# Optimization experiments

Measured on AMD Instinct MI355X. Metric: run time of the kernel, lower is better.

Reference implementation:

```python
import jax, jax.numpy as jnp
import numpy as np

N_ATT, N_HEAD, D_K, D_IN = 4, 8, 64, 512
B, T = 128, 512
TEMP = float(np.sqrt(D_K))  # temperature = d_k ** 0.5


def setup_inputs() -> dict:
    key = jax.random.key(0)
    k1, k2, k3 = jax.random.split(key, 3)
    v = jax.random.normal(k1, (B, T, D_IN), jnp.float32)
    # nn.Parameter Q init: normal(0, sqrt(2/d_k))
    Q = jax.random.normal(k2, (N_ATT, N_HEAD, D_K), jnp.float32) * np.sqrt(2.0 / D_K)
    # fc1_k: Linear(d_in, num_attention*n_head*d_k), weight ~ N(0, sqrt(2/d_k))
    Wk = jax.random.normal(k3, (N_ATT * N_HEAD * D_K, D_IN), jnp.float32) * np.sqrt(2.0 / D_K)
    bk = jnp.zeros((N_ATT * N_HEAD * D_K,), jnp.float32)
    return {"v": v, "Q": Q, "Wk": Wk, "bk": bk}


def reference(v, Q, Wk, bk):
    A, H, dk = Q.shape
    Bsz, Tt, d_in = v.shape
    c = d_in // H  # per-head value channels

    # q = stack(Q, dim=2 over batch).view(-1, d_k)  -> [A*H*B, d_k]
    q = jnp.broadcast_to(Q[:, :, None, :], (A, H, Bsz, dk)).reshape(-1, dk)

    # k = fc1_k(v).view(B,T,A,H,dk).permute(3,0,1,2,4).contiguous().view(-1,T,dk)
    # NOTE: this view is a raw C-order reinterpretation (scrambles t/A axes);
    # transpose + reshape reproduces torch's contiguous().view() exactly.
    k = (v @ Wk.T + bk).reshape(Bsz, Tt, A, H, dk)
    k = jnp.transpose(k, (3, 0, 1, 2, 4)).reshape(-1, Tt, dk)  # [H*B*A, T, dk]

    # v heads: stack(v.split(c, dim=-1)).view(H*B, T, c)
    vh = jnp.transpose(v.reshape(Bsz, Tt, H, c), (2, 0, 1, 3)).reshape(H * Bsz, Tt, c)

    # single-query scaled dot-product attention (dropout in eval mode -> identity)
    attn = jnp.einsum('xd,xtd->xt', q, k) / TEMP  # [A*H*B, T]
    attn = jax.nn.softmax(attn, axis=-1)

    # v[:, None].expand(-1, A, -1, -1).reshape(-1, T, c)
    vexp = jnp.broadcast_to(vh[:, None], (H * Bsz, A, Tt, c)).reshape(-1, Tt, c)
    out = jnp.einsum('xt,xtc->xc', attn, vexp)  # [A*H*B, c]

    output = out.reshape(A, H, Bsz, c)
    attn = attn.reshape(A, H, Bsz, Tt)
    return output, attn
```

## Files before the change

kernel.cpp:

```cpp
#include <hip/hip_runtime.h>
#include <hip/hip_bf16.h>
#include <math.h>

#define DIN 512
#define TT  512

using bf16x8 = __attribute__((ext_vector_type(8))) short;
using f32x4  = __attribute__((ext_vector_type(4))) float;

static __device__ __forceinline__ unsigned short f2bf(float x) {
    __hip_bfloat16 h = __float2bfloat16(x);
    return *reinterpret_cast<unsigned short*>(&h);
}
static __device__ __forceinline__ unsigned int pack2(float a, float b) {
    return (unsigned int)f2bf(a) | ((unsigned int)f2bf(b) << 16);
}


__global__ __launch_bounds__(512) void pk_kernel(const float* __restrict__ Q,
                                                 const float* __restrict__ Wk,
                                                 const float* __restrict__ bk,
                                                 unsigned short* __restrict__ Pgb,
                                                 float* __restrict__ qb) {
    const int bid = blockIdx.x;
    const int bg = bid >> 5;
    const int p  = bid & 31;
    const int h  = p >> 2;
    const int ua = p & 3;
    const int a_q = h >> 1;
    const int h_q = (4 * h + bg) & 7;
    const int ch_base = ua * 512 + h * 64;

    __shared__ float qv[64];
    const int tid = threadIdx.x;
    if (tid < 64) qv[tid] = Q[(a_q * 8 + h_q) * 64 + tid];
    __syncthreads();

    const int s = tid;
    float acc = 0.f;
    #pragma unroll 8
    for (int d = 0; d < 64; ++d)
        acc += qv[d] * Wk[(size_t)(ch_base + d) * DIN + s];
    Pgb[(size_t)(bg * 32 + p) * 512 + s] = f2bf(acc * 0.125f);

    if (tid == 0) {
        float sum = 0.f;
        for (int d = 0; d < 64; ++d) sum += qv[d] * bk[ch_base + d];
        qb[bg * 32 + p] = sum * 0.125f;
    }
}

__global__ __launch_bounds__(256) void score_kernel(const float* __restrict__ v,
                                                    const unsigned short* __restrict__ Pgb,
                                                    const float* __restrict__ qb,
                                                    float* __restrict__ attn) {
    const int bid = blockIdx.x;
    const int b = bid >> 2;
    const int j = bid & 3;
    const int bg = b >> 5;
    const int tid = threadIdx.x;
    const int lane = tid & 63;
    const int w = tid >> 6;

    __shared__ __align__(16) char VtB[2][128 * 80];
    __shared__ float red2[4][2][4][2];

    const float* vbase = v + ((size_t)b * TT + j * 128) * DIN;
    const int srow  = tid >> 1;
    const int shalf = tid & 1;
    const float* vsrc = vbase + (size_t)srow * DIN + shalf * 16;
    const int vdo = srow * 80 + shalf * 32;

    const unsigned short* pb0 = Pgb + ((size_t)(bg * 32) + (lane & 15)) * 512 + (lane >> 4) * 8;
    const unsigned short* pb1 = pb0 + 16 * 512;

    const int akb = (lane >> 4) * 16;
    const int aoff = (w * 32 + (lane & 15)) * 80 + akb;

    const float qv0 = qb[bg * 32 + (lane & 15)];
    const float qv1 = qb[bg * 32 + 16 + (lane & 15)];

    f32x4 acc[2][2];
    #pragma unroll
    for (int i = 0; i < 2; ++i)
        #pragma unroll
        for (int n = 0; n < 2; ++n)
            #pragma unroll
            for (int r = 0; r < 4; ++r) acc[i][n][r] = 0.f;

    float4 vrA[4], vrB[4];
    bf16x8 brA0, brA1, brB0, brB1;
    #pragma unroll
    for (int q = 0; q < 4; ++q) vrA[q] = *(const float4*)(vsrc + q * 4);
    brA0 = *(const bf16x8*)(pb0);
    brA1 = *(const bf16x8*)(pb1);
    {
        uint4 lo, hi;
        lo.x = pack2(vrA[0].x, vrA[0].y); lo.y = pack2(vrA[0].z, vrA[0].w);
        lo.z = pack2(vrA[1].x, vrA[1].y); lo.w = pack2(vrA[1].z, vrA[1].w);
        hi.x = pack2(vrA[2].x, vrA[2].y); hi.y = pack2(vrA[2].z, vrA[2].w);
        hi.z = pack2(vrA[3].x, vrA[3].y); hi.w = pack2(vrA[3].z, vrA[3].w);
        *(uint4*)(VtB[0] + vdo)      = lo;
        *(uint4*)(VtB[0] + vdo + 16) = hi;
    }
    __syncthreads();

#define STEP(CUR, VRN, BRC0, BRC1, BRN0, BRN1, KT)                            \
    {                                                                         \
        if ((KT) + 1 < 16) {                                                  \
            const float* vn = vsrc + ((KT) + 1) * 32;                         \
            VRN[0] = *(const float4*)(vn);                                    \
            VRN[1] = *(const float4*)(vn + 4);                                \
            VRN[2] = *(const float4*)(vn + 8);                                \
            VRN[3] = *(const float4*)(vn + 12);                               \
            BRN0 = *(const bf16x8*)(pb0 + ((KT) + 1) * 32);                   \
            BRN1 = *(const bf16x8*)(pb1 + ((KT) + 1) * 32);                   \
        }                                                                     \
        bf16x8 a0 = *(const bf16x8*)(VtB[CUR] + aoff);                        \
        bf16x8 a1 = *(const bf16x8*)(VtB[CUR] + aoff + 16 * 80);              \
        acc[0][0] = __builtin_amdgcn_mfma_f32_16x16x32_bf16(a0, BRC0, acc[0][0], 0, 0, 0); \
        acc[0][1] = __builtin_amdgcn_mfma_f32_16x16x32_bf16(a0, BRC1, acc[0][1], 0, 0, 0); \
        acc[1][0] = __builtin_amdgcn_mfma_f32_16x16x32_bf16(a1, BRC0, acc[1][0], 0, 0, 0); \
        acc[1][1] = __builtin_amdgcn_mfma_f32_16x16x32_bf16(a1, BRC1, acc[1][1], 0, 0, 0); \
        if ((KT) + 1 < 16) {                                                  \
            uint4 lo, hi;                                                     \
            lo.x = pack2(VRN[0].x, VRN[0].y); lo.y = pack2(VRN[0].z, VRN[0].w); \
            lo.z = pack2(VRN[1].x, VRN[1].y); lo.w = pack2(VRN[1].z, VRN[1].w); \
            hi.x = pack2(VRN[2].x, VRN[2].y); hi.y = pack2(VRN[2].z, VRN[2].w); \
            hi.z = pack2(VRN[3].x, VRN[3].y); hi.w = pack2(VRN[3].z, VRN[3].w); \
            *(uint4*)(VtB[(CUR) ^ 1] + vdo)      = lo;                        \
            *(uint4*)(VtB[(CUR) ^ 1] + vdo + 16) = hi;                        \
        }                                                                     \
        __syncthreads();                                                      \
    }

    for (int kt = 0; kt < 16; kt += 2) {
        STEP(0, vrB, brA0, brA1, brB0, brB1, kt)
        STEP(1, vrA, brB0, brB1, brA0, brA1, kt + 1)
    }
#undef STEP

    float lg[2][8];
    #pragma unroll
    for (int i = 0; i < 2; ++i)
        #pragma unroll
        for (int r = 0; r < 4; ++r) {
            lg[0][i * 4 + r] = acc[i][0][r] + qv0;
            lg[1][i * 4 + r] = acc[i][1][r] + qv1;
        }

    const int hsub = (lane >> 2) & 3;
    float mw[2], sw[2], ev[2][8];
    #pragma unroll
    for (int nt = 0; nt < 2; ++nt) {
        float m = lg[nt][0];
        #pragma unroll
        for (int q = 1; q < 8; ++q) m = fmaxf(m, lg[nt][q]);
        m = fmaxf(m, __shfl_xor(m, 1));
        m = fmaxf(m, __shfl_xor(m, 2));
        m = fmaxf(m, __shfl_xor(m, 16));
        m = fmaxf(m, __shfl_xor(m, 32));
        float s = 0.f;
        #pragma unroll
        for (int q = 0; q < 8; ++q) { ev[nt][q] = __expf(lg[nt][q] - m); s += ev[nt][q]; }
        s += __shfl_xor(s, 1);
        s += __shfl_xor(s, 2);
        s += __shfl_xor(s, 16);
        s += __shfl_xor(s, 32);
        mw[nt] = m; sw[nt] = s;
    }
    if ((lane & 0x33) == 0) {
        #pragma unroll
        for (int nt = 0; nt < 2; ++nt) {
            red2[w][nt][hsub][0] = mw[nt];
            red2[w][nt][hsub][1] = sw[nt];
        }
    }
    __syncthreads();

    #pragma unroll
    for (int nt = 0; nt < 2; ++nt) {
        float M = red2[0][nt][hsub][0];
        M = fmaxf(M, red2[1][nt][hsub][0]);
        M = fmaxf(M, red2[2][nt][hsub][0]);
        M = fmaxf(M, red2[3][nt][hsub][0]);
        float S = 0.f;
        #pragma unroll
        for (int w2 = 0; w2 < 4; ++w2)
            S += __expf(red2[w2][nt][hsub][0] - M) * red2[w2][nt][hsub][1];
        const float factor = __expf(mw[nt] - M) / S;

        const int h = nt * 4 + hsub;
        float* arow = attn + ((size_t)(h * 512 + b * 4 + j)) * 512;
        const int ua = lane & 3;
        #pragma unroll
        for (int i = 0; i < 2; ++i)
            #pragma unroll
            for (int r = 0; r < 4; ++r) {
                const int trow = w * 32 + i * 16 + ((lane >> 4) & 3) * 4 + r;
                arow[trow * 4 + ua] = ev[nt][i * 4 + r] * factor;
            }
    }
}

__global__ __launch_bounds__(256) void pv_kernel(const float* __restrict__ v,
                                                 const float* __restrict__ attn,
                                                 float* __restrict__ out) {
    const int bid = blockIdx.x;
    const int b = bid >> 3;
    const int h = bid & 7;
    const int tid = threadIdx.x;

    __shared__ __align__(16) char smem[34816];
    float (*at)[512]    = reinterpret_cast<float (*)[512]>(smem);
    float (*red)[4][68] = reinterpret_cast<float (*)[4][68]>(smem);

    {
        const int j  = tid >> 6;
        const int u8 = (tid & 63) * 8;
        const float* src = attn + ((size_t)(h * 512 + b * 4 + j)) * 512 + u8;
        *(float4*)&at[j][u8]     = *(const float4*)(src);
        *(float4*)&at[j][u8 + 4] = *(const float4*)(src + 4);
    }
    __syncthreads();

    const int cg = tid & 7;
    const int up = tid >> 3;
    const int c8 = cg * 8;
    const float* vb = v + (size_t)b * TT * DIN + h * 64 + c8;

    float acc[4][8];
    #pragma unroll
    for (int jj = 0; jj < 4; ++jj)
        #pragma unroll
        for (int ci = 0; ci < 8; ++ci) acc[jj][ci] = 0.f;

    float4 r0 = *(const float4*)(vb + (size_t)up * DIN);
    float4 r1 = *(const float4*)(vb + (size_t)up * DIN + 4);

    for (int it = 0; it < 16; ++it) {
        const int u = it * 32 + up;
        const float4 c0 = r0;
        const float4 c1 = r1;
        if (it < 15) {
            const float* pn = vb + (size_t)(u + 32) * DIN;
            r0 = *(const float4*)(pn);
            r1 = *(const float4*)(pn + 4);
        }
        const float a0 = at[0][u];
        const float a1 = at[1][u];
        const float a2 = at[2][u];
        const float a3 = at[3][u];
        acc[0][0] += a0 * c0.x; acc[0][1] += a0 * c0.y; acc[0][2] += a0 * c0.z; acc[0][3] += a0 * c0.w;
        acc[0][4] += a0 * c1.x; acc[0][5] += a0 * c1.y; acc[0][6] += a0 * c1.z; acc[0][7] += a0 * c1.w;
        acc[1][0] += a1 * c0.x; acc[1][1] += a1 * c0.y; acc[1][2] += a1 * c0.z; acc[1][3] += a1 * c0.w;
        acc[1][4] += a1 * c1.x; acc[1][5] += a1 * c1.y; acc[1][6] += a1 * c1.z; acc[1][7] += a1 * c1.w;
        acc[2][0] += a2 * c0.x; acc[2][1] += a2 * c0.y; acc[2][2] += a2 * c0.z; acc[2][3] += a2 * c0.w;
        acc[2][4] += a2 * c1.x; acc[2][5] += a2 * c1.y; acc[2][6] += a2 * c1.z; acc[2][7] += a2 * c1.w;
        acc[3][0] += a3 * c0.x; acc[3][1] += a3 * c0.y; acc[3][2] += a3 * c0.z; acc[3][3] += a3 * c0.w;
        acc[3][4] += a3 * c1.x; acc[3][5] += a3 * c1.y; acc[3][6] += a3 * c1.z; acc[3][7] += a3 * c1.w;
    }

    __syncthreads();

    #pragma unroll
    for (int jj = 0; jj < 4; ++jj) {
        float4 w0, w1;
        w0.x = acc[jj][0]; w0.y = acc[jj][1]; w0.z = acc[jj][2]; w0.w = acc[jj][3];
        w1.x = acc[jj][4]; w1.y = acc[jj][5]; w1.z = acc[jj][6]; w1.w = acc[jj][7];
        *(float4*)&red[up][jj][c8]     = w0;
        *(float4*)&red[up][jj][c8 + 4] = w1;
    }
    __syncthreads();

    const int jo = tid >> 6;
    const int c  = tid & 63;
    float s = 0.f;
    #pragma unroll
    for (int r2 = 0; r2 < 32; ++r2) s += red[r2][jo][c];
    out[((size_t)(h * 512 + b * 4 + jo)) * 64 + c] = s;
}

extern "C" void kernel_launch(void* const* d_in, const int* in_sizes, int n_in,
                              void* d_out, int out_size, void* d_ws, size_t ws_size,
                              hipStream_t stream) {
    const float* v  = (const float*)d_in[0];
    const float* Q  = (const float*)d_in[1];
    const float* Wk = (const float*)d_in[2];
    const float* bk = (const float*)d_in[3];

    float* out  = (float*)d_out;
    float* attn = out + 4096 * 64;

    unsigned short* Pgb = (unsigned short*)d_ws;
    float* qb = (float*)(Pgb + 4 * 32 * 512);

    pk_kernel<<<128, 512, 0, stream>>>(Q, Wk, bk, Pgb, qb);
    score_kernel<<<512, 256, 0, stream>>>(v, Pgb, qb, attn);
    pv_kernel<<<1024, 256, 0, stream>>>(v, attn, out);
}
```

Measured before the change: 59.17 us.

## Fuse score and PV kernels into persistent work-queue kernel with per-batch flags

```diff
diff --git a/kernel.cpp b/kernel.cpp
--- a/kernel.cpp
+++ b/kernel.cpp
@@ -21,7 +21,9 @@
                                                  const float* __restrict__ Wk,
                                                  const float* __restrict__ bk,
                                                  unsigned short* __restrict__ Pgb,
-                                                 float* __restrict__ qb) {
+                                                 float* __restrict__ qb,
+                                                 int* __restrict__ flags,
+                                                 int* __restrict__ ctr) {
     const int bid = blockIdx.x;
     const int bg = bid >> 5;
     const int p  = bid & 31;
@@ -34,6 +36,10 @@
     __shared__ float qv[64];
     const int tid = threadIdx.x;
     if (tid < 64) qv[tid] = Q[(a_q * 8 + h_q) * 64 + tid];
+    if (tid == 0) {
+        flags[bid] = 0;
+        if (bid == 0) *ctr = 0;
+    }
     __syncthreads();
 
     const int s = tid;
@@ -50,60 +56,75 @@
     }
 }
 
-__global__ __launch_bounds__(256) void score_kernel(const float* __restrict__ v,
-                                                    const unsigned short* __restrict__ Pgb,
-                                                    const float* __restrict__ qb,
-                                                    float* __restrict__ attn) {
-    const int bid = blockIdx.x;
-    const int b = bid >> 2;
-    const int j = bid & 3;
-    const int bg = b >> 5;
-    const int tid = threadIdx.x;
+__global__ __launch_bounds__(256, 3) void persist_kernel(
+        const float* __restrict__ v,
+        const unsigned short* __restrict__ Pgb,
+        const float* __restrict__ qb,
+        float* __restrict__ attn,
+        float* __restrict__ out,
+        int* __restrict__ flags,
+        int* __restrict__ ctr)
+{
+    __shared__ __align__(16) char smem[34816];
+    __shared__ int s_item;
+    const int tid  = threadIdx.x;
     const int lane = tid & 63;
-    const int w = tid >> 6;
-
-    __shared__ __align__(16) char VtB[2][128 * 80];
-    __shared__ float red2[4][2][4][2];
-
-    const float* vbase = v + ((size_t)b * TT + j * 128) * DIN;
-    const int srow  = tid >> 1;
-    const int shalf = tid & 1;
-    const float* vsrc = vbase + (size_t)srow * DIN + shalf * 16;
-    const int vdo = srow * 80 + shalf * 32;
-
-    const unsigned short* pb0 = Pgb + ((size_t)(bg * 32) + (lane & 15)) * 512 + (lane >> 4) * 8;
-    const unsigned short* pb1 = pb0 + 16 * 512;
-
-    const int akb = (lane >> 4) * 16;
-    const int aoff = (w * 32 + (lane & 15)) * 80 + akb;
-
-    const float qv0 = qb[bg * 32 + (lane & 15)];
-    const float qv1 = qb[bg * 32 + 16 + (lane & 15)];
-
-    f32x4 acc[2][2];
-    #pragma unroll
-    for (int i = 0; i < 2; ++i)
-        #pragma unroll
-        for (int n = 0; n < 2; ++n)
-            #pragma unroll
-            for (int r = 0; r < 4; ++r) acc[i][n][r] = 0.f;
-
-    float4 vrA[4], vrB[4];
-    bf16x8 brA0, brA1, brB0, brB1;
-    #pragma unroll
-    for (int q = 0; q < 4; ++q) vrA[q] = *(const float4*)(vsrc + q * 4);
-    brA0 = *(const bf16x8*)(pb0);
-    brA1 = *(const bf16x8*)(pb1);
-    {
-        uint4 lo, hi;
-        lo.x = pack2(vrA[0].x, vrA[0].y); lo.y = pack2(vrA[0].z, vrA[0].w);
-        lo.z = pack2(vrA[1].x, vrA[1].y); lo.w = pack2(vrA[1].z, vrA[1].w);
-        hi.x = pack2(vrA[2].x, vrA[2].y); hi.y = pack2(vrA[2].z, vrA[2].w);
-        hi.z = pack2(vrA[3].x, vrA[3].y); hi.w = pack2(vrA[3].z, vrA[3].w);
-        *(uint4*)(VtB[0] + vdo)      = lo;
-        *(uint4*)(VtB[0] + vdo + 16) = hi;
-    }
-    __syncthreads();
+    const int w    = tid >> 6;
+
+    for (;;) {
+        __syncthreads();
+        if (tid == 0) s_item = atomicAdd(ctr, 1);
+        __syncthreads();
+        const int item = s_item;
+        if (item >= 1536) break;
+
+        if (item < 512) {
+            const int b = item >> 2;
+            const int j = item & 3;
+            const int bg = b >> 5;
+
+            char* vt[2] = { smem, smem + 10240 };
+            float (*red2)[2][4][2] = reinterpret_cast<float (*)[2][4][2]>(smem + 20480);
+
+            const float* vbase = v + ((size_t)b * TT + j * 128) * DIN;
+            const int srow  = tid >> 1;
+            const int shalf = tid & 1;
+            const float* vsrc = vbase + (size_t)srow * DIN + shalf * 16;
+            const int vdo = srow * 80 + shalf * 32;
+
+            const unsigned short* pb0 = Pgb + ((size_t)(bg * 32) + (lane & 15)) * 512 + (lane >> 4) * 8;
+            const unsigned short* pb1 = pb0 + 16 * 512;
+
+            const int akb  = (lane >> 4) * 16;
+            const int aoff = (w * 32 + (lane & 15)) * 80 + akb;
+
+            const float qv0 = qb[bg * 32 + (lane & 15)];
+            const float qv1 = qb[bg * 32 + 16 + (lane & 15)];
+
+            f32x4 acc[2][2];
+            #pragma unroll
+            for (int i = 0; i < 2; ++i)
+                #pragma unroll
+                for (int n = 0; n < 2; ++n)
+                    #pragma unroll
+                    for (int r = 0; r < 4; ++r) acc[i][n][r] = 0.f;
+
+            float4 vrA[4], vrB[4];
+            bf16x8 brA0, brA1, brB0, brB1;
+            #pragma unroll
+            for (int q = 0; q < 4; ++q) vrA[q] = *(const float4*)(vsrc + q * 4);
+            brA0 = *(const bf16x8*)(pb0);
+            brA1 = *(const bf16x8*)(pb1);
+            {
+                uint4 lo, hi;
+                lo.x = pack2(vrA[0].x, vrA[0].y); lo.y = pack2(vrA[0].z, vrA[0].w);
+                lo.z = pack2(vrA[1].x, vrA[1].y); lo.w = pack2(vrA[1].z, vrA[1].w);
+                hi.x = pack2(vrA[2].x, vrA[2].y); hi.y = pack2(vrA[2].z, vrA[2].w);
+                hi.z = pack2(vrA[3].x, vrA[3].y); hi.w = pack2(vrA[3].z, vrA[3].w);
+                *(uint4*)(vt[0] + vdo)      = lo;
+                *(uint4*)(vt[0] + vdo + 16) = hi;
+            }
+            __syncthreads();
 
 #define STEP(CUR, VRN, BRC0, BRC1, BRN0, BRN1, KT)                            \
     {                                                                         \
@@ -116,8 +137,8 @@
             BRN0 = *(const bf16x8*)(pb0 + ((KT) + 1) * 32);                   \
             BRN1 = *(const bf16x8*)(pb1 + ((KT) + 1) * 32);                   \
         }                                                                     \
-        bf16x8 a0 = *(const bf16x8*)(VtB[CUR] + aoff);                        \
-        bf16x8 a1 = *(const bf16x8*)(VtB[CUR] + aoff + 16 * 80);              \
+        bf16x8 a0 = *(const bf16x8*)(vt[CUR] + aoff);                         \
+        bf16x8 a1 = *(const bf16x8*)(vt[CUR] + aoff + 16 * 80);               \
         acc[0][0] = __builtin_amdgcn_mfma_f32_16x16x32_bf16(a0, BRC0, acc[0][0], 0, 0, 0); \
         acc[0][1] = __builtin_amdgcn_mfma_f32_16x16x32_bf16(a0, BRC1, acc[0][1], 0, 0, 0); \
         acc[1][0] = __builtin_amdgcn_mfma_f32_16x16x32_bf16(a1, BRC0, acc[1][0], 0, 0, 0); \
@@ -128,157 +149,164 @@
             lo.z = pack2(VRN[1].x, VRN[1].y); lo.w = pack2(VRN[1].z, VRN[1].w); \
             hi.x = pack2(VRN[2].x, VRN[2].y); hi.y = pack2(VRN[2].z, VRN[2].w); \
             hi.z = pack2(VRN[3].x, VRN[3].y); hi.w = pack2(VRN[3].z, VRN[3].w); \
-            *(uint4*)(VtB[(CUR) ^ 1] + vdo)      = lo;                        \
-            *(uint4*)(VtB[(CUR) ^ 1] + vdo + 16) = hi;                        \
+            *(uint4*)(vt[(CUR) ^ 1] + vdo)      = lo;                         \
+            *(uint4*)(vt[(CUR) ^ 1] + vdo + 16) = hi;                         \
         }                                                                     \
         __syncthreads();                                                      \
     }
 
-    for (int kt = 0; kt < 16; kt += 2) {
-        STEP(0, vrB, brA0, brA1, brB0, brB1, kt)
-        STEP(1, vrA, brB0, brB1, brA0, brA1, kt + 1)
-    }
+            for (int kt = 0; kt < 16; kt += 2) {
+                STEP(0, vrB, brA0, brA1, brB0, brB1, kt)
+                STEP(1, vrA, brB0, brB1, brA0, brA1, kt + 1)
+            }
 #undef STEP
 
-    float lg[2][8];
-    #pragma unroll
-    for (int i = 0; i < 2; ++i)
-        #pragma unroll
-        for (int r = 0; r < 4; ++r) {
-            lg[0][i * 4 + r] = acc[i][0][r] + qv0;
-            lg[1][i * 4 + r] = acc[i][1][r] + qv1;
-        }
-
-    const int hsub = (lane >> 2) & 3;
-    float mw[2], sw[2], ev[2][8];
-    #pragma unroll
-    for (int nt = 0; nt < 2; ++nt) {
-        float m = lg[nt][0];
-        #pragma unroll
-        for (int q = 1; q < 8; ++q) m = fmaxf(m, lg[nt][q]);
-        m = fmaxf(m, __shfl_xor(m, 1));
-        m = fmaxf(m, __shfl_xor(m, 2));
-        m = fmaxf(m, __shfl_xor(m, 16));
-        m = fmaxf(m, __shfl_xor(m, 32));
-        float s = 0.f;
-        #pragma unroll
-        for (int q = 0; q < 8; ++q) { ev[nt][q] = __expf(lg[nt][q] - m); s += ev[nt][q]; }
-        s += __shfl_xor(s, 1);
-        s += __shfl_xor(s, 2);
-        s += __shfl_xor(s, 16);
-        s += __shfl_xor(s, 32);
-        mw[nt] = m; sw[nt] = s;
-    }
-    if ((lane & 0x33) == 0) {
-        #pragma unroll
-        for (int nt = 0; nt < 2; ++nt) {
-            red2[w][nt][hsub][0] = mw[nt];
-            red2[w][nt][hsub][1] = sw[nt];
+            float lg[2][8];
+            #pragma unroll
+            for (int i = 0; i < 2; ++i)
+                #pragma unroll
+                for (int r = 0; r < 4; ++r) {
+                    lg[0][i * 4 + r] = acc[i][0][r] + qv0;
+                    lg[1][i * 4 + r] = acc[i][1][r] + qv1;
+                }
+
+            const int hsub = (lane >> 2) & 3;
+            float mw[2], sw[2], ev[2][8];
+            #pragma unroll
+            for (int nt = 0; nt < 2; ++nt) {
+                float m = lg[nt][0];
+                #pragma unroll
+                for (int q = 1; q < 8; ++q) m = fmaxf(m, lg[nt][q]);
+                m = fmaxf(m, __shfl_xor(m, 1));
+                m = fmaxf(m, __shfl_xor(m, 2));
+                m = fmaxf(m, __shfl_xor(m, 16));
+                m = fmaxf(m, __shfl_xor(m, 32));
+                float s = 0.f;
+                #pragma unroll
+                for (int q = 0; q < 8; ++q) { ev[nt][q] = __expf(lg[nt][q] - m); s += ev[nt][q]; }
+                s += __shfl_xor(s, 1);
+                s += __shfl_xor(s, 2);
+                s += __shfl_xor(s, 16);
+                s += __shfl_xor(s, 32);
+                mw[nt] = m; sw[nt] = s;
+            }
+            if ((lane & 0x33) == 0) {
+                #pragma unroll
+                for (int nt = 0; nt < 2; ++nt) {
+                    red2[w][nt][hsub][0] = mw[nt];
+                    red2[w][nt][hsub][1] = sw[nt];
+                }
+            }
+            __syncthreads();
+
+            #pragma unroll
+            for (int nt = 0; nt < 2; ++nt) {
+                float M = red2[0][nt][hsub][0];
+                M = fmaxf(M, red2[1][nt][hsub][0]);
+                M = fmaxf(M, red2[2][nt][hsub][0]);
+                M = fmaxf(M, red2[3][nt][hsub][0]);
+                float S = 0.f;
+                #pragma unroll
+                for (int w2 = 0; w2 < 4; ++w2)
+                    S += __expf(red2[w2][nt][hsub][0] - M) * red2[w2][nt][hsub][1];
+                const float factor = __expf(mw[nt] - M) / S;
+
+                const int h = nt * 4 + hsub;
+                float* arow = attn + ((size_t)(h * 512 + b * 4 + j)) * 512;
+                const int ua = lane & 3;
+                #pragma unroll
+                for (int i = 0; i < 2; ++i)
+                    #pragma unroll
+                    for (int r = 0; r < 4; ++r) {
+                        const int trow = w * 32 + i * 16 + ((lane >> 4) & 3) * 4 + r;
+                        arow[trow * 4 + ua] = ev[nt][i * 4 + r] * factor;
+                    }
+            }
+
+            __syncthreads();
+            if (tid == 0)
+                __hip_atomic_fetch_add(flags + b, 1, __ATOMIC_RELEASE, __HIP_MEMORY_SCOPE_AGENT);
+
+        } else {
+            const int t = item - 512;
+            const int b = t >> 3;
+            const int h = t & 7;
+
+            if (tid == 0) {
+                while (__hip_atomic_load(flags + b, __ATOMIC_ACQUIRE, __HIP_MEMORY_SCOPE_AGENT) < 4)
+                    __builtin_amdgcn_s_sleep(2);
+            }
+            __syncthreads();
+
+            float (*at)[512]    = reinterpret_cast<float (*)[512]>(smem);
+            float (*red)[4][68] = reinterpret_cast<float (*)[4][68]>(smem);
+
+            {
+                const int jj = tid >> 6;
+                const int u8 = (tid & 63) * 8;
+                const float* src = attn + ((size_t)(h * 512 + b * 4 + jj)) * 512 + u8;
+                *(float4*)&at[jj][u8]     = *(const float4*)(src);
+                *(float4*)&at[jj][u8 + 4] = *(const float4*)(src + 4);
+            }
+            __syncthreads();
+
+            const int cg = tid & 7;
+            const int up = tid >> 3;
+            const int c8 = cg * 8;
+            const float* vb = v + (size_t)b * TT * DIN + h * 64 + c8;
+
+            float acc[4][8];
+            #pragma unroll
+            for (int jj = 0; jj < 4; ++jj)
+                #pragma unroll
+                for (int ci = 0; ci < 8; ++ci) acc[jj][ci] = 0.f;
+
+            float4 r0 = *(const float4*)(vb + (size_t)up * DIN);
+            float4 r1 = *(const float4*)(vb + (size_t)up * DIN + 4);
+
+            for (int it2 = 0; it2 < 16; ++it2) {
+                const int u = it2 * 32 + up;
+                const float4 c0 = r0;
+                const float4 c1 = r1;
+                if (it2 < 15) {
+                    const float* pn = vb + (size_t)(u + 32) * DIN;
+                    r0 = *(const float4*)(pn);
+                    r1 = *(const float4*)(pn + 4);
+                }
+                const float a0 = at[0][u];
+                const float a1 = at[1][u];
+                const float a2 = at[2][u];
+                const float a3 = at[3][u];
+                acc[0][0] += a0 * c0.x; acc[0][1] += a0 * c0.y; acc[0][2] += a0 * c0.z; acc[0][3] += a0 * c0.w;
+                acc[0][4] += a0 * c1.x; acc[0][5] += a0 * c1.y; acc[0][6] += a0 * c1.z; acc[0][7] += a0 * c1.w;
+                acc[1][0] += a1 * c0.x; acc[1][1] += a1 * c0.y; acc[1][2] += a1 * c0.z; acc[1][3] += a1 * c0.w;
+                acc[1][4] += a1 * c1.x; acc[1][5] += a1 * c1.y; acc[1][6] += a1 * c1.z; acc[1][7] += a1 * c1.w;
+                acc[2][0] += a2 * c0.x; acc[2][1] += a2 * c0.y; acc[2][2] += a2 * c0.z; acc[2][3] += a2 * c0.w;
+                acc[2][4] += a2 * c1.x; acc[2][5] += a2 * c1.y; acc[2][6] += a2 * c1.z; acc[2][7] += a2 * c1.w;
+                acc[3][0] += a3 * c0.x; acc[3][1] += a3 * c0.y; acc[3][2] += a3 * c0.z; acc[3][3] += a3 * c0.w;
+                acc[3][4] += a3 * c1.x; acc[3][5] += a3 * c1.y; acc[3][6] += a3 * c1.z; acc[3][7] += a3 * c1.w;
+            }
+
+            __syncthreads();
+
+            #pragma unroll
+            for (int jj = 0; jj < 4; ++jj) {
+                float4 w0, w1;
+                w0.x = acc[jj][0]; w0.y = acc[jj][1]; w0.z = acc[jj][2]; w0.w = acc[jj][3];
+                w1.x = acc[jj][4]; w1.y = acc[jj][5]; w1.z = acc[jj][6]; w1.w = acc[jj][7];
+                *(float4*)&red[up][jj][c8]     = w0;
+                *(float4*)&red[up][jj][c8 + 4] = w1;
+            }
+            __syncthreads();
+
+            const int jo = tid >> 6;
+            const int c  = tid & 63;
+            float s = 0.f;
+            #pragma unroll
+            for (int r2 = 0; r2 < 32; ++r2) s += red[r2][jo][c];
+            out[((size_t)(h * 512 + b * 4 + jo)) * 64 + c] = s;
         }
     }
-    __syncthreads();
-
-    #pragma unroll
-    for (int nt = 0; nt < 2; ++nt) {
-        float M = red2[0][nt][hsub][0];
-        M = fmaxf(M, red2[1][nt][hsub][0]);
-        M = fmaxf(M, red2[2][nt][hsub][0]);
-        M = fmaxf(M, red2[3][nt][hsub][0]);
-        float S = 0.f;
-        #pragma unroll
-        for (int w2 = 0; w2 < 4; ++w2)
-            S += __expf(red2[w2][nt][hsub][0] - M) * red2[w2][nt][hsub][1];
-        const float factor = __expf(mw[nt] - M) / S;
-
-        const int h = nt * 4 + hsub;
-        float* arow = attn + ((size_t)(h * 512 + b * 4 + j)) * 512;
-        const int ua = lane & 3;
-        #pragma unroll
-        for (int i = 0; i < 2; ++i)
-            #pragma unroll
-            for (int r = 0; r < 4; ++r) {
-                const int trow = w * 32 + i * 16 + ((lane >> 4) & 3) * 4 + r;
-                arow[trow * 4 + ua] = ev[nt][i * 4 + r] * factor;
-            }
-    }
-}
-
-__global__ __launch_bounds__(256) void pv_kernel(const float* __restrict__ v,
-                                                 const float* __restrict__ attn,
-                                                 float* __restrict__ out) {
-    const int bid = blockIdx.x;
-    const int b = bid >> 3;
-    const int h = bid & 7;
-    const int tid = threadIdx.x;
-
-    __shared__ __align__(16) char smem[34816];
-    float (*at)[512]    = reinterpret_cast<float (*)[512]>(smem);
-    float (*red)[4][68] = reinterpret_cast<float (*)[4][68]>(smem);
-
-    {
-        const int j  = tid >> 6;
-        const int u8 = (tid & 63) * 8;
-        const float* src = attn + ((size_t)(h * 512 + b * 4 + j)) * 512 + u8;
-        *(float4*)&at[j][u8]     = *(const float4*)(src);
-        *(float4*)&at[j][u8 + 4] = *(const float4*)(src + 4);
-    }
-    __syncthreads();
-
-    const int cg = tid & 7;
-    const int up = tid >> 3;
-    const int c8 = cg * 8;
-    const float* vb = v + (size_t)b * TT * DIN + h * 64 + c8;
-
-    float acc[4][8];
-    #pragma unroll
-    for (int jj = 0; jj < 4; ++jj)
-        #pragma unroll
-        for (int ci = 0; ci < 8; ++ci) acc[jj][ci] = 0.f;
-
-    float4 r0 = *(const float4*)(vb + (size_t)up * DIN);
-    float4 r1 = *(const float4*)(vb + (size_t)up * DIN + 4);
-
-    for (int it = 0; it < 16; ++it) {
-        const int u = it * 32 + up;
-        const float4 c0 = r0;
-        const float4 c1 = r1;
-        if (it < 15) {
-            const float* pn = vb + (size_t)(u + 32) * DIN;
-            r0 = *(const float4*)(pn);
-            r1 = *(const float4*)(pn + 4);
-        }
-        const float a0 = at[0][u];
-        const float a1 = at[1][u];
-        const float a2 = at[2][u];
-        const float a3 = at[3][u];
-        acc[0][0] += a0 * c0.x; acc[0][1] += a0 * c0.y; acc[0][2] += a0 * c0.z; acc[0][3] += a0 * c0.w;
-        acc[0][4] += a0 * c1.x; acc[0][5] += a0 * c1.y; acc[0][6] += a0 * c1.z; acc[0][7] += a0 * c1.w;
-        acc[1][0] += a1 * c0.x; acc[1][1] += a1 * c0.y; acc[1][2] += a1 * c0.z; acc[1][3] += a1 * c0.w;
-        acc[1][4] += a1 * c1.x; acc[1][5] += a1 * c1.y; acc[1][6] += a1 * c1.z; acc[1][7] += a1 * c1.w;
-        acc[2][0] += a2 * c0.x; acc[2][1] += a2 * c0.y; acc[2][2] += a2 * c0.z; acc[2][3] += a2 * c0.w;
-        acc[2][4] += a2 * c1.x; acc[2][5] += a2 * c1.y; acc[2][6] += a2 * c1.z; acc[2][7] += a2 * c1.w;
-        acc[3][0] += a3 * c0.x; acc[3][1] += a3 * c0.y; acc[3][2] += a3 * c0.z; acc[3][3] += a3 * c0.w;
-        acc[3][4] += a3 * c1.x; acc[3][5] += a3 * c1.y; acc[3][6] += a3 * c1.z; acc[3][7] += a3 * c1.w;
-    }
-
-    __syncthreads();
-
-    #pragma unroll
-    for (int jj = 0; jj < 4; ++jj) {
-        float4 w0, w1;
-        w0.x = acc[jj][0]; w0.y = acc[jj][1]; w0.z = acc[jj][2]; w0.w = acc[jj][3];
-        w1.x = acc[jj][4]; w1.y = acc[jj][5]; w1.z = acc[jj][6]; w1.w = acc[jj][7];
-        *(float4*)&red[up][jj][c8]     = w0;
-        *(float4*)&red[up][jj][c8 + 4] = w1;
-    }
-    __syncthreads();
-
-    const int jo = tid >> 6;
-    const int c  = tid & 63;
-    float s = 0.f;
-    #pragma unroll
-    for (int r2 = 0; r2 < 32; ++r2) s += red[r2][jo][c];
-    out[((size_t)(h * 512 + b * 4 + jo)) * 64 + c] = s;
 }
 
 extern "C" void kernel_launch(void* const* d_in, const int* in_sizes, int n_in,
@@ -293,9 +321,10 @@
     float* attn = out + 4096 * 64;
 
     unsigned short* Pgb = (unsigned short*)d_ws;
-    float* qb = (float*)(Pgb + 4 * 32 * 512);
-
-    pk_kernel<<<128, 512, 0, stream>>>(Q, Wk, bk, Pgb, qb);
-    score_kernel<<<512, 256, 0, stream>>>(v, Pgb, qb, attn);
-    pv_kernel<<<1024, 256, 0, stream>>>(v, attn, out);
-}
+    float* qb  = (float*)(Pgb + 4 * 32 * 512);
+    int* flags = (int*)(qb + 128);
+    int* ctr   = flags + 128;
+
+    pk_kernel<<<128, 512, 0, stream>>>(Q, Wk, bk, Pgb, qb, flags, ctr);
+    persist_kernel<<<1024, 256, 0, stream>>>(v, Pgb, qb, attn, out, flags, ctr);
+}
```

Result: slower. 159.9 us (+170.2%).
